# Optimization experiments

Hardware: AMD Instinct MI355X
Metric: run time of the kernel (lower is better)

## Reference

```python
import jax, jax.numpy as jnp
import numpy as np

N_EMBD = 2048
H_I = 16   # indexer heads
D_I = 32   # indexer dim


def setup_inputs() -> dict:
    key = jax.random.key(0)
    k1, k2, k3, k4 = jax.random.split(key, 4)
    x = jax.random.normal(k1, (2, 4096, N_EMBD), dtype=jnp.float32)
    # nn.Linear(in, out, bias=False) weights, stored (out, in) like torch
    s = 1.0 / np.sqrt(N_EMBD)
    Wq = jax.random.uniform(k2, (H_I * D_I, N_EMBD), jnp.float32, -s, s)
    Wk = jax.random.uniform(k3, (D_I, N_EMBD), jnp.float32, -s, s)
    Ww = jax.random.uniform(k4, (H_I, N_EMBD), jnp.float32, -s, s)
    return {"x": x, "Wq": Wq, "Wk": Wk, "Ww": Ww}


def reference(x, Wq, Wk, Ww):
    B, T, C = x.shape
    q = (x @ Wq.T).reshape(B, T, H_I, D_I)   # (B,T,H,D)
    k = x @ Wk.T                              # (B,T,D)
    w = x @ Ww.T                              # (B,T,H)
    scores = jnp.einsum('bqhd,bkd->bqhk', q, k)
    scores = jax.nn.relu(scores)
    importance = jnp.einsum('bqh,bqhk->bqk', w, scores)  # (B,T,T)
    return importance
```

## Files before the change

kernel.cpp:

```cpp
#include <hip/hip_runtime.h>
#include <hip/hip_bf16.h>
#include <stdint.h>


typedef __attribute__((ext_vector_type(8))) short bf16x8;
typedef __attribute__((ext_vector_type(4))) float f32x4;

#define NPAD 640
#define KCOL 512
#define WCOL 544

__device__ __forceinline__ unsigned short f2bf(float f) {
  union { float f; unsigned u; } c; c.f = f;
  unsigned u = c.u;
  u += 0x7FFFu + ((u >> 16) & 1u);
  return (unsigned short)(u >> 16);
}

__device__ __forceinline__ void async_copy16(void* lds, const void* g) {
  __builtin_amdgcn_global_load_lds(
      (const __attribute__((address_space(1))) unsigned*)g,
      (__attribute__((address_space(3))) unsigned*)lds, 16, 0, 0);
}

__global__ __launch_bounds__(256) void pack_kernel(
    const float* __restrict__ x, const float* __restrict__ Wq,
    const float* __restrict__ Wk, const float* __restrict__ Ww,
    unsigned short* __restrict__ xb, unsigned short* __restrict__ Wp) {
  const int64_t NX4 = 16777216 / 4;
  int64_t i = (int64_t)blockIdx.x * 256 + threadIdx.x;
  if (i < NX4) {
    float4 v = ((const float4*)x)[i];
    ushort4 o;
    o.x = f2bf(v.x); o.y = f2bf(v.y); o.z = f2bf(v.z); o.w = f2bf(v.w);
    ((ushort4*)xb)[i] = o;
  } else {
    int p = (int)(i - NX4);
    int row = p >> 9;
    int col = (p & 511) << 2;
    float4 v = make_float4(0.f, 0.f, 0.f, 0.f);
    if (row < 512)      v = *(const float4*)(Wq + (int64_t)row * 2048 + col);
    else if (row < 544) v = *(const float4*)(Wk + (int64_t)(row - 512) * 2048 + col);
    else if (row < 560) v = *(const float4*)(Ww + (int64_t)(row - 544) * 2048 + col);
    ushort4 o;
    o.x = f2bf(v.x); o.y = f2bf(v.y); o.z = f2bf(v.z); o.w = f2bf(v.w);
    ((ushort4*)Wp)[p] = o;
  }
}

__global__ __launch_bounds__(256) void gemm_proj(
    const unsigned short* __restrict__ xb, const unsigned short* __restrict__ Wp,
    unsigned short* __restrict__ qkwb, float* __restrict__ wf) {
  __shared__ short lds_a[128 * 32];
  __shared__ short lds_b[128 * 32];
  const int tid = threadIdx.x;
  const int lane = tid & 63;
  const int l15 = lane & 15, quad = lane >> 4;
  const int wave = tid >> 6;
  const int wm = wave >> 1, wn = wave & 1;
  const int m0 = blockIdx.y * 128, n0 = blockIdx.x * 128;

  const int c0 = tid, c1 = tid + 256;
  const unsigned short* ga0 = xb + (int64_t)(m0 + (c0 >> 2)) * 2048 + (c0 & 3) * 8;
  const unsigned short* ga1 = xb + (int64_t)(m0 + (c1 >> 2)) * 2048 + (c1 & 3) * 8;
  const unsigned short* gb0 = Wp + (int64_t)(n0 + (c0 >> 2)) * 2048 + (c0 & 3) * 8;
  const unsigned short* gb1 = Wp + (int64_t)(n0 + (c1 >> 2)) * 2048 + (c1 & 3) * 8;

  f32x4 acc[4][4] = {};

  for (int kt = 0; kt < 64; ++kt) {
    const int ko = kt * 32;
    async_copy16(&lds_a[c0 * 8], ga0 + ko);
    async_copy16(&lds_a[c1 * 8], ga1 + ko);
    async_copy16(&lds_b[c0 * 8], gb0 + ko);
    async_copy16(&lds_b[c1 * 8], gb1 + ko);
    __syncthreads();
    bf16x8 af[4], bfr[4];
#pragma unroll
    for (int i = 0; i < 4; ++i)
      af[i] = *(const bf16x8*)&lds_a[(wm * 64 + i * 16 + l15) * 32 + quad * 8];
#pragma unroll
    for (int j = 0; j < 4; ++j)
      bfr[j] = *(const bf16x8*)&lds_b[(wn * 64 + j * 16 + l15) * 32 + quad * 8];
#pragma unroll
    for (int i = 0; i < 4; ++i)
#pragma unroll
      for (int j = 0; j < 4; ++j)
        acc[i][j] = __builtin_amdgcn_mfma_f32_16x16x32_bf16(af[i], bfr[j], acc[i][j], 0, 0, 0);
    __syncthreads();
  }

#pragma unroll
  for (int i = 0; i < 4; ++i)
#pragma unroll
    for (int j = 0; j < 4; ++j)
#pragma unroll
      for (int r = 0; r < 4; ++r) {
        int m = m0 + wm * 64 + i * 16 + quad * 4 + r;
        int n = n0 + wn * 64 + j * 16 + l15;
        float v = acc[i][j][r];
        qkwb[(int64_t)m * NPAD + n] = f2bf(v);
        if (n >= WCOL && n < WCOL + 16) wf[m * 16 + (n - WCOL)] = v;
      }
}

__global__ __launch_bounds__(256) void scores_kernel(
    const unsigned short* __restrict__ qkwb, const float* __restrict__ wf,
    float* __restrict__ out) {
  const int kt = blockIdx.x, qt = blockIdx.y, b = blockIdx.z;
  const int tid = threadIdx.x;
  const int lane = tid & 63;
  const int l15 = lane & 15, quad = lane >> 4;
  const int wave = tid >> 6;
  const int wk = wave & 1, wq = wave >> 1;

  __shared__ float w_lds[16][132];

  const int qrow0 = b * 4096 + qt * 128;
  const int krow0 = b * 4096 + kt * 128;

  {
    const float4* ws = (const float4*)(wf + (int64_t)qrow0 * 16);
#pragma unroll
    for (int r = 0; r < 2; ++r) {
      int f = tid * 2 + r;
      float4 v = ws[f];
      int row = f >> 2, hb = (f & 3) * 4;
      w_lds[hb + 0][row] = v.x; w_lds[hb + 1][row] = v.y;
      w_lds[hb + 2][row] = v.z; w_lds[hb + 3][row] = v.w;
    }
  }

  bf16x8 ka[4];
#pragma unroll
  for (int i = 0; i < 4; ++i) {
    int kk = krow0 + wk * 64 + i * 16 + l15;
    ka[i] = *(const bf16x8*)&qkwb[(int64_t)kk * NPAD + KCOL + quad * 8];
  }

  const unsigned short* qbase =
      qkwb + (int64_t)(qrow0 + wq * 64 + l15) * NPAD + quad * 8;

  f32x4 acc[4][4] = {};
  __syncthreads();

  bf16x8 qc[4], qn[4];
#pragma unroll
  for (int j = 0; j < 4; ++j) qc[j] = *(const bf16x8*)&qbase[(int64_t)j * 16 * NPAD];

  for (int h = 0; h < 16; ++h) {
    if (h < 15) {
#pragma unroll
      for (int j = 0; j < 4; ++j)
        qn[j] = *(const bf16x8*)&qbase[(int64_t)j * 16 * NPAD + (h + 1) * 32];
    }
    float wv[4];
#pragma unroll
    for (int j = 0; j < 4; ++j) wv[j] = w_lds[h][wq * 64 + j * 16 + l15];
#pragma unroll
    for (int i = 0; i < 4; ++i)
#pragma unroll
      for (int j = 0; j < 4; ++j) {
        f32x4 z = {0.f, 0.f, 0.f, 0.f};
        f32x4 t = __builtin_amdgcn_mfma_f32_16x16x32_bf16(ka[i], qc[j], z, 0, 0, 0);
#pragma unroll
        for (int r = 0; r < 4; ++r)
          acc[i][j][r] += fmaxf(t[r], 0.f) * wv[j];
      }
#pragma unroll
    for (int j = 0; j < 4; ++j) qc[j] = qn[j];
  }

#pragma unroll
  for (int i = 0; i < 4; ++i)
#pragma unroll
    for (int j = 0; j < 4; ++j) {
      int q = qt * 128 + wq * 64 + j * 16 + l15;
      int k = kt * 128 + wk * 64 + i * 16 + quad * 4;
      float4 v = make_float4(acc[i][j][0], acc[i][j][1], acc[i][j][2], acc[i][j][3]);
      *(float4*)&out[((int64_t)b * 4096 + q) * 4096 + k] = v;
    }
}

extern "C" void kernel_launch(void* const* d_in, const int* in_sizes, int n_in,
                              void* d_out, int out_size, void* d_ws, size_t ws_size,
                              hipStream_t stream) {
  const float* x  = (const float*)d_in[0];
  const float* Wq = (const float*)d_in[1];
  const float* Wk = (const float*)d_in[2];
  const float* Ww = (const float*)d_in[3];
  float* out = (float*)d_out;

  char* ws = (char*)d_ws;
  unsigned short* xb   = (unsigned short*)ws;
  unsigned short* Wp   = (unsigned short*)(ws + 33554432);
  unsigned short* qkwb = (unsigned short*)(ws + 36175872);
  float*          wf   = (float*)(ws + 46661632);

  pack_kernel<<<17664, 256, 0, stream>>>(x, Wq, Wk, Ww, xb, Wp);
  gemm_proj<<<dim3(5, 64), 256, 0, stream>>>(xb, Wp, qkwb, wf);
  scores_kernel<<<dim3(32, 32, 2), 256, 0, stream>>>(qkwb, wf, out);
}
```

Before: 303.6 us.

## Use relu(x)=(x+|x|)/2 identity to fold linear term into precombined query

Rewrites relu as half of (t + |t|). The linear half is precomputed by a new combine kernel that forms a per-token weighted sum of q over heads (w/2 times q), which seeds the accumulator with a single MFMA per tile. The per-head inner loop then becomes a single fmaf on fabs, with the 0.5 folded into the stored w. The projection GEMM is retiled to 128x64 tiles with a 64-wide K step, the padded width is shrunk to 576 columns, and the head loop is unrolled by two with double-buffered q fragments. This adds a kernel launch and extra bf16 rounding of the combined query, in exchange for cheaper per-element epilogue math and less padded projection work.

```diff
diff --git a/kernel.cpp b/kernel.cpp
--- a/kernel.cpp
+++ b/kernel.cpp
@@ -6,7 +6,7 @@
 typedef __attribute__((ext_vector_type(8))) short bf16x8;
 typedef __attribute__((ext_vector_type(4))) float f32x4;
 
-#define NPAD 640
+#define NPAD 576
 #define KCOL 512
 #define WCOL 544
 
@@ -16,7 +16,10 @@
   u += 0x7FFFu + ((u >> 16) & 1u);
   return (unsigned short)(u >> 16);
 }
-
+__device__ __forceinline__ float bf2f(unsigned short u) {
+  union { unsigned u; float f; } c; c.u = ((unsigned)u) << 16;
+  return c.f;
+}
 __device__ __forceinline__ void async_copy16(void* lds, const void* g) {
   __builtin_amdgcn_global_load_lds(
       (const __attribute__((address_space(1))) unsigned*)g,
@@ -51,63 +54,95 @@
 __global__ __launch_bounds__(256) void gemm_proj(
     const unsigned short* __restrict__ xb, const unsigned short* __restrict__ Wp,
     unsigned short* __restrict__ qkwb, float* __restrict__ wf) {
-  __shared__ short lds_a[128 * 32];
-  __shared__ short lds_b[128 * 32];
+  __shared__ short lA[2 * 128 * 32];
+  __shared__ short lB[2 * 64 * 32];
   const int tid = threadIdx.x;
   const int lane = tid & 63;
   const int l15 = lane & 15, quad = lane >> 4;
-  const int wave = tid >> 6;
-  const int wm = wave >> 1, wn = wave & 1;
-  const int m0 = blockIdx.y * 128, n0 = blockIdx.x * 128;
-
-  const int c0 = tid, c1 = tid + 256;
-  const unsigned short* ga0 = xb + (int64_t)(m0 + (c0 >> 2)) * 2048 + (c0 & 3) * 8;
-  const unsigned short* ga1 = xb + (int64_t)(m0 + (c1 >> 2)) * 2048 + (c1 & 3) * 8;
-  const unsigned short* gb0 = Wp + (int64_t)(n0 + (c0 >> 2)) * 2048 + (c0 & 3) * 8;
-  const unsigned short* gb1 = Wp + (int64_t)(n0 + (c1 >> 2)) * 2048 + (c1 & 3) * 8;
-
-  f32x4 acc[4][4] = {};
-
-  for (int kt = 0; kt < 64; ++kt) {
-    const int ko = kt * 32;
-    async_copy16(&lds_a[c0 * 8], ga0 + ko);
-    async_copy16(&lds_a[c1 * 8], ga1 + ko);
-    async_copy16(&lds_b[c0 * 8], gb0 + ko);
-    async_copy16(&lds_b[c1 * 8], gb1 + ko);
+  const int wm = tid >> 6;
+  const int n0 = blockIdx.x * 64, m0 = blockIdx.y * 128;
+
+  const unsigned short* gA[4];
+  const unsigned short* gB[2];
+  int cA[4], cB[2];
+#pragma unroll
+  for (int u = 0; u < 4; ++u) {
+    int c = tid + u * 256;
+    cA[u] = c;
+    int kh = c >> 9, row = (c >> 2) & 127, cc = c & 3;
+    gA[u] = xb + (int64_t)(m0 + row) * 2048 + kh * 32 + cc * 8;
+  }
+#pragma unroll
+  for (int u = 0; u < 2; ++u) {
+    int c = tid + u * 256;
+    cB[u] = c;
+    int kh = c >> 8, row = (c >> 2) & 63, cc = c & 3;
+    gB[u] = Wp + (int64_t)(n0 + row) * 2048 + kh * 32 + cc * 8;
+  }
+
+  f32x4 acc[2][4] = {};
+
+  for (int kt = 0; kt < 32; ++kt) {
+    const int ko = kt * 64;
+#pragma unroll
+    for (int u = 0; u < 4; ++u) async_copy16(&lA[cA[u] * 8], gA[u] + ko);
+#pragma unroll
+    for (int u = 0; u < 2; ++u) async_copy16(&lB[cB[u] * 8], gB[u] + ko);
     __syncthreads();
-    bf16x8 af[4], bfr[4];
-#pragma unroll
-    for (int i = 0; i < 4; ++i)
-      af[i] = *(const bf16x8*)&lds_a[(wm * 64 + i * 16 + l15) * 32 + quad * 8];
+#pragma unroll
+    for (int ks = 0; ks < 2; ++ks) {
+      bf16x8 af[2], bfr[4];
+#pragma unroll
+      for (int i = 0; i < 2; ++i)
+        af[i] = *(const bf16x8*)&lA[(ks * 128 + wm * 32 + i * 16 + l15) * 32 + quad * 8];
+#pragma unroll
+      for (int j = 0; j < 4; ++j)
+        bfr[j] = *(const bf16x8*)&lB[(ks * 64 + j * 16 + l15) * 32 + quad * 8];
+#pragma unroll
+      for (int i = 0; i < 2; ++i)
+#pragma unroll
+        for (int j = 0; j < 4; ++j)
+          acc[i][j] = __builtin_amdgcn_mfma_f32_16x16x32_bf16(af[i], bfr[j], acc[i][j], 0, 0, 0);
+    }
+    __syncthreads();
+  }
+
+#pragma unroll
+  for (int i = 0; i < 2; ++i)
 #pragma unroll
     for (int j = 0; j < 4; ++j)
-      bfr[j] = *(const bf16x8*)&lds_b[(wn * 64 + j * 16 + l15) * 32 + quad * 8];
-#pragma unroll
-    for (int i = 0; i < 4; ++i)
-#pragma unroll
-      for (int j = 0; j < 4; ++j)
-        acc[i][j] = __builtin_amdgcn_mfma_f32_16x16x32_bf16(af[i], bfr[j], acc[i][j], 0, 0, 0);
-    __syncthreads();
-  }
-
-#pragma unroll
-  for (int i = 0; i < 4; ++i)
-#pragma unroll
-    for (int j = 0; j < 4; ++j)
 #pragma unroll
       for (int r = 0; r < 4; ++r) {
-        int m = m0 + wm * 64 + i * 16 + quad * 4 + r;
-        int n = n0 + wn * 64 + j * 16 + l15;
+        int m = m0 + wm * 32 + i * 16 + quad * 4 + r;
+        int n = n0 + j * 16 + l15;
         float v = acc[i][j][r];
         qkwb[(int64_t)m * NPAD + n] = f2bf(v);
-        if (n >= WCOL && n < WCOL + 16) wf[m * 16 + (n - WCOL)] = v;
+        if (n >= WCOL && n < WCOL + 16) wf[m * 16 + (n - WCOL)] = 0.5f * v;
       }
+}
+
+__global__ __launch_bounds__(256) void combine_kernel(
+    const unsigned short* __restrict__ qkwb, const float* __restrict__ wf,
+    unsigned short* __restrict__ qt) {
+  int gid = blockIdx.x * 256 + threadIdx.x;
+  int m = gid >> 3, dq = (gid & 7) * 4;
+  const unsigned short* qrow = qkwb + (int64_t)m * NPAD + dq;
+  float s0 = 0, s1 = 0, s2 = 0, s3 = 0;
+#pragma unroll
+  for (int h = 0; h < 16; ++h) {
+    ushort4 qv = *(const ushort4*)(qrow + h * 32);
+    float u = wf[m * 16 + h];
+    s0 += u * bf2f(qv.x); s1 += u * bf2f(qv.y);
+    s2 += u * bf2f(qv.z); s3 += u * bf2f(qv.w);
+  }
+  ushort4 o; o.x = f2bf(s0); o.y = f2bf(s1); o.z = f2bf(s2); o.w = f2bf(s3);
+  *(ushort4*)(qt + (int64_t)m * 32 + dq) = o;
 }
 
 __global__ __launch_bounds__(256) void scores_kernel(
     const unsigned short* __restrict__ qkwb, const float* __restrict__ wf,
-    float* __restrict__ out) {
-  const int kt = blockIdx.x, qt = blockIdx.y, b = blockIdx.z;
+    const unsigned short* __restrict__ qt, float* __restrict__ out) {
+  const int kt = blockIdx.x, qtile = blockIdx.y, b = blockIdx.z;
   const int tid = threadIdx.x;
   const int lane = tid & 63;
   const int l15 = lane & 15, quad = lane >> 4;
@@ -116,7 +151,7 @@
 
   __shared__ float w_lds[16][132];
 
-  const int qrow0 = b * 4096 + qt * 128;
+  const int qrow0 = b * 4096 + qtile * 128;
   const int krow0 = b * 4096 + kt * 128;
 
   {
@@ -138,44 +173,60 @@
     ka[i] = *(const bf16x8*)&qkwb[(int64_t)kk * NPAD + KCOL + quad * 8];
   }
 
+  const f32x4 z0 = {0.f, 0.f, 0.f, 0.f};
+
+  f32x4 acc[4][4];
+  {
+#pragma unroll
+    for (int j = 0; j < 4; ++j) {
+      bf16x8 qtf = *(const bf16x8*)&qt[(int64_t)(qrow0 + wq * 64 + j * 16 + l15) * 32 + quad * 8];
+#pragma unroll
+      for (int i = 0; i < 4; ++i)
+        acc[i][j] = __builtin_amdgcn_mfma_f32_16x16x32_bf16(ka[i], qtf, z0, 0, 0, 0);
+    }
+  }
+
   const unsigned short* qbase =
       qkwb + (int64_t)(qrow0 + wq * 64 + l15) * NPAD + quad * 8;
 
-  f32x4 acc[4][4] = {};
+  bf16x8 qa[4], qb[4];
+#pragma unroll
+  for (int j = 0; j < 4; ++j) qa[j] = *(const bf16x8*)&qbase[(int64_t)j * 16 * NPAD];
+
   __syncthreads();
 
-  bf16x8 qc[4], qn[4];
-#pragma unroll
-  for (int j = 0; j < 4; ++j) qc[j] = *(const bf16x8*)&qbase[(int64_t)j * 16 * NPAD];
-
-  for (int h = 0; h < 16; ++h) {
-    if (h < 15) {
+#define SCORE_BODY(QF, H)                                                      \
+  {                                                                            \
+    float wv[4];                                                               \
+    _Pragma("unroll") for (int j = 0; j < 4; ++j)                              \
+        wv[j] = w_lds[H][wq * 64 + j * 16 + l15];                              \
+    _Pragma("unroll") for (int i = 0; i < 4; ++i)                              \
+    _Pragma("unroll") for (int j = 0; j < 4; ++j) {                            \
+      f32x4 t = __builtin_amdgcn_mfma_f32_16x16x32_bf16(ka[i], QF[j], z0, 0, 0, 0); \
+      _Pragma("unroll") for (int r = 0; r < 4; ++r)                            \
+          acc[i][j][r] = fmaf(wv[j], fabsf(t[r]), acc[i][j][r]);               \
+    }                                                                          \
+  }
+
+  for (int h = 0; h < 16; h += 2) {
+#pragma unroll
+    for (int j = 0; j < 4; ++j)
+      qb[j] = *(const bf16x8*)&qbase[(int64_t)j * 16 * NPAD + (h + 1) * 32];
+    SCORE_BODY(qa, h)
+    if (h + 2 < 16) {
 #pragma unroll
       for (int j = 0; j < 4; ++j)
-        qn[j] = *(const bf16x8*)&qbase[(int64_t)j * 16 * NPAD + (h + 1) * 32];
-    }
-    float wv[4];
-#pragma unroll
-    for (int j = 0; j < 4; ++j) wv[j] = w_lds[h][wq * 64 + j * 16 + l15];
-#pragma unroll
-    for (int i = 0; i < 4; ++i)
-#pragma unroll
-      for (int j = 0; j < 4; ++j) {
-        f32x4 z = {0.f, 0.f, 0.f, 0.f};
-        f32x4 t = __builtin_amdgcn_mfma_f32_16x16x32_bf16(ka[i], qc[j], z, 0, 0, 0);
-#pragma unroll
-        for (int r = 0; r < 4; ++r)
-          acc[i][j][r] += fmaxf(t[r], 0.f) * wv[j];
-      }
-#pragma unroll
-    for (int j = 0; j < 4; ++j) qc[j] = qn[j];
-  }
+        qa[j] = *(const bf16x8*)&qbase[(int64_t)j * 16 * NPAD + (h + 2) * 32];
+    }
+    SCORE_BODY(qb, h + 1)
+  }
+#undef SCORE_BODY
 
 #pragma unroll
   for (int i = 0; i < 4; ++i)
 #pragma unroll
     for (int j = 0; j < 4; ++j) {
-      int q = qt * 128 + wq * 64 + j * 16 + l15;
+      int q = qtile * 128 + wq * 64 + j * 16 + l15;
       int k = kt * 128 + wk * 64 + i * 16 + quad * 4;
       float4 v = make_float4(acc[i][j][0], acc[i][j][1], acc[i][j][2], acc[i][j][3]);
       *(float4*)&out[((int64_t)b * 4096 + q) * 4096 + k] = v;
@@ -194,10 +245,12 @@
   char* ws = (char*)d_ws;
   unsigned short* xb   = (unsigned short*)ws;
   unsigned short* Wp   = (unsigned short*)(ws + 33554432);
-  unsigned short* qkwb = (unsigned short*)(ws + 36175872);
-  float*          wf   = (float*)(ws + 46661632);
-
-  pack_kernel<<<17664, 256, 0, stream>>>(x, Wq, Wk, Ww, xb, Wp);
-  gemm_proj<<<dim3(5, 64), 256, 0, stream>>>(xb, Wp, qkwb, wf);
-  scores_kernel<<<dim3(32, 32, 2), 256, 0, stream>>>(qkwb, wf, out);
-}
+  unsigned short* qkwb = (unsigned short*)(ws + 35913728);
+  float*          wf   = (float*)(ws + 45350912);
+  unsigned short* qt   = (unsigned short*)(ws + 45875200);
+
+  pack_kernel<<<17536, 256, 0, stream>>>(x, Wq, Wk, Ww, xb, Wp);
+  gemm_proj<<<dim3(9, 64), 256, 0, stream>>>(xb, Wp, qkwb, wf);
+  combine_kernel<<<256, 256, 0, stream>>>(qkwb, wf, qt);
+  scores_kernel<<<dim3(32, 32, 2), 256, 0, stream>>>(qkwb, wf, qt, out);
+}
```

New measurement: 713.0 us. +134.8%, slower.
